# Optimization experiments

Hardware: AMD Instinct MI355X
Metric: run time of the kernel (lower is better)

## Reference

```python
import jax, jax.numpy as jnp
import numpy as np

B, LATENT = 8192, 1024
NR, NC = 12, 12                      # nb_rows, nb_cols
H0, W0 = NR + 2, NC + 2              # 14x14 after reshape
EPS = 1e-5
SLOPE = 0.01                         # LeakyReLU default


def setup_inputs() -> dict:
    key = jax.random.key(0)
    ks = jax.random.split(key, 9)
    s = 0.05
    return {
        "x": jax.random.normal(ks[0], (B, LATENT), jnp.float32),
        "fc_w": jax.random.normal(ks[1], (H0 * W0 * 36, LATENT), jnp.float32) * s,
        "fc_b": jax.random.normal(ks[2], (H0 * W0 * 36,), jnp.float32) * s,
        "conv_w": jax.random.normal(ks[3], (16, 36, 2, 2), jnp.float32) * s,
        "conv_b": jax.random.normal(ks[4], (16,), jnp.float32) * s,
        "gamma": jnp.ones((16,), jnp.float32),
        "beta": jnp.zeros((16,), jnp.float32),
        # locally-connected weights: (out_ch, in_ch, Hout, Wout, k*k)
        "lw1": jax.random.normal(ks[5], (6, 16, H0 - 1, W0 - 1, 4), jnp.float32) * s,
        "lw2": jax.random.normal(ks[6], (1, 6, H0 - 2, W0 - 2, 4), jnp.float32) * s,
    }


def _leaky(x):
    return jnp.where(x >= 0, x, SLOPE * x)


def _local_conv2(x, w):
    # x: (B,C,H,W); w: (O,C,Ho,Wo,4) with k=2, stride 1, no padding
    Ho, Wo = w.shape[2], w.shape[3]
    patches = jnp.stack(
        [x[:, :, dy:dy + Ho, dx:dx + Wo] for dy in (0, 1) for dx in (0, 1)],
        axis=-1)  # (B,C,Ho,Wo,4)
    return jnp.einsum('bchwk,ochwk->bohw', patches, w)


def reference(x, fc_w, fc_b, conv_w, conv_b, gamma, beta, lw1, lw2):
    # fc -> view(B, H0, W0, 36) -> permute to NCHW
    h = x @ fc_w.T + fc_b
    h = h.reshape(B, H0, W0, 36).transpose(0, 3, 1, 2)  # (B,36,14,14)
    # Conv2d k=2 padding='same' (torch pads bottom/right for even kernels)
    h = jax.lax.conv_general_dilated(
        h, conv_w, window_strides=(1, 1), padding=((0, 1), (0, 1)),
        dimension_numbers=('NCHW', 'OIHW', 'NCHW')) + conv_b[None, :, None, None]
    h = _leaky(h)
    # BatchNorm2d (training mode: batch stats, biased var)
    mu = h.mean(axis=(0, 2, 3), keepdims=True)
    var = h.var(axis=(0, 2, 3), keepdims=True)
    h = (h - mu) * jax.lax.rsqrt(var + EPS)
    h = h * gamma[None, :, None, None] + beta[None, :, None, None]
    # locally-connected stack: 14x14 -> 13x13 -> 12x12
    h = _leaky(_local_conv2(h, lw1))
    return _local_conv2(h, lw2)  # (B,1,12,12)
```

## Files before the change

kernel.cpp:

```cpp
#include <hip/hip_runtime.h>


#define SLOPE 0.01f

typedef __bf16 bf16x8 __attribute__((ext_vector_type(8)));
typedef float f32x4 __attribute__((ext_vector_type(4)));

typedef const __attribute__((address_space(1))) void* gas_ptr;
typedef __attribute__((address_space(3))) void* las_ptr;

__device__ __forceinline__ void load16_to_lds(const void* g, void* l) {
  __builtin_amdgcn_global_load_lds((gas_ptr)g, (las_ptr)l, 16, 0, 0);
}

__device__ __forceinline__ unsigned short f2bf(float f) {
  union { float f; unsigned int u; } v; v.f = f;
  unsigned int r = v.u + 0x7FFFu + ((v.u >> 16) & 1u);
  return (unsigned short)(r >> 16);
}
__device__ __forceinline__ float bfbits2f(unsigned int bits16) {
  union { unsigned int u; float f; } v; v.u = bits16 << 16;
  return v.f;
}
__device__ __forceinline__ float leaky(float v) { return v >= 0.f ? v : SLOPE * v; }

__global__ void k_cast_x(const float* __restrict__ x, unsigned short* __restrict__ xb,
                         float* __restrict__ stats) {
  if (blockIdx.x == 0 && threadIdx.x < 32) stats[threadIdx.x] = 0.f;
  int gid = blockIdx.x * 256 + threadIdx.x;
  const float4* x4 = (const float4*)x;
  float4 a = x4[gid * 2], b = x4[gid * 2 + 1];
  union { unsigned short s[8]; uint4 v; } o;
  o.s[0] = f2bf(a.x); o.s[1] = f2bf(a.y); o.s[2] = f2bf(a.z); o.s[3] = f2bf(a.w);
  o.s[4] = f2bf(b.x); o.s[5] = f2bf(b.y); o.s[6] = f2bf(b.z); o.s[7] = f2bf(b.w);
  ((uint4*)xb)[gid] = o.v;
}

__global__ void k_fold(const float* __restrict__ fc_w, const float* __restrict__ fc_b,
                       const float* __restrict__ conv_w, const float* __restrict__ conv_b,
                       unsigned short* __restrict__ Wc, float* __restrict__ bc) {
  __shared__ __align__(16) float cwm[2304];
  int blk = blockIdx.x, t = threadIdx.x;
  if (blk == 196) {
    uint4 z = make_uint4(0, 0, 0, 0);
    uint4* dst = (uint4*)(Wc + 3136 * 1024);
    for (int i = t; i < 8192; i += 256) dst[i] = z;
    for (int i = 3136 + t; i < 3200; i += 256) bc[i] = 0.f;
    return;
  }
  int i0 = blk / 14, j0 = blk - (blk / 14) * 14;
  float m[4];
  int rb[4];
#pragma unroll
  for (int kk = 0; kk < 4; kk++) {
    int dy = kk >> 1, dx = kk & 1;
    int ii = i0 + dy, jj = j0 + dx;
    m[kk] = (ii <= 13 && jj <= 13) ? 1.f : 0.f;
    int iic = ii > 13 ? 13 : ii, jjc = jj > 13 ? 13 : jj;
    rb[kk] = (iic * 14 + jjc) * 36;
  }
  for (int i = t; i < 2304; i += 256) cwm[i] = conv_w[i] * m[i & 3];
  __syncthreads();

  f32x4 acc[16];
#pragma unroll
  for (int o = 0; o < 16; o++) acc[o] = (f32x4){0.f, 0.f, 0.f, 0.f};
  const int kc4 = t * 4;
#pragma unroll 2
  for (int c = 0; c < 36; c++) {
    f32x4 f0 = *(const f32x4*)(fc_w + (rb[0] + c) * 1024 + kc4);
    f32x4 f1 = *(const f32x4*)(fc_w + (rb[1] + c) * 1024 + kc4);
    f32x4 f2 = *(const f32x4*)(fc_w + (rb[2] + c) * 1024 + kc4);
    f32x4 f3 = *(const f32x4*)(fc_w + (rb[3] + c) * 1024 + kc4);
#pragma unroll
    for (int o = 0; o < 16; o++) {
      f32x4 wv = *(const f32x4*)(cwm + (o * 36 + c) * 4);
      acc[o] += wv.x * f0 + wv.y * f1 + wv.z * f2 + wv.w * f3;
    }
  }
#pragma unroll
  for (int o = 0; o < 16; o++) {
    int n = o * 196 + i0 * 14 + j0;
    union { unsigned short s[4]; uint2 v; } u;
    u.s[0] = f2bf(acc[o][0]); u.s[1] = f2bf(acc[o][1]);
    u.s[2] = f2bf(acc[o][2]); u.s[3] = f2bf(acc[o][3]);
    *(uint2*)(Wc + n * 1024 + kc4) = u.v;
  }
  if (t < 16) {
    int o = t;
    float b = conv_b[o];
    for (int c = 0; c < 36; c++)
      for (int dy = 0; dy < 2; dy++) {
        int ii = i0 + dy; if (ii > 13) continue;
        for (int dx = 0; dx < 2; dx++) {
          int jj = j0 + dx; if (jj > 13) continue;
          b += conv_w[(o * 36 + c) * 4 + dy * 2 + dx] * fc_b[(ii * 14 + jj) * 36 + c];
        }
      }
    bc[o * 196 + i0 * 14 + j0] = b;
  }
}

__global__ __launch_bounds__(256, 4) void k_gemm(const unsigned short* __restrict__ Xb,
                                                 const unsigned short* __restrict__ Wcb,
                                                 const float* __restrict__ bc,
                                                 unsigned short* __restrict__ h2,
                                                 float* __restrict__ stats) {
  __shared__ __align__(16) char lds[16384];
  __shared__ float red[4][4];
  const int t = threadIdx.x;
  const int w = t >> 6, lane = t & 63;
  const int quad = lane >> 4, l15 = lane & 15;
  const int bid = blockIdx.x;
  const int xcd = bid & 7, j = bid >> 3;
  const int mblk = xcd * 8 + (j & 7);
  const int nblk = j >> 3;
  const int m0 = mblk * 128, n0 = nblk * 128;
  const int mrow = t & 127, tko = t >> 7;
  const unsigned short* ga = Xb + (m0 + mrow) * 1024 + tko * 8;
  const unsigned short* gb = Wcb + (n0 + mrow) * 1024 + tko * 8;
  char* lA = lds;
  char* lB = lds + 8192;
  const int wbase = w * 1024;
  const int wm0 = (w >> 1) * 64, wn0 = (w & 1) * 64;

  f32x4 acc[4][4];
#pragma unroll
  for (int a = 0; a < 4; a++)
#pragma unroll
    for (int b = 0; b < 4; b++) acc[a][b] = (f32x4){0.f, 0.f, 0.f, 0.f};

  for (int kb = 0; kb < 1024; kb += 32) {
    __syncthreads();
    load16_to_lds(ga + kb,      lA + wbase);
    load16_to_lds(ga + kb + 16, lA + 4096 + wbase);
    load16_to_lds(gb + kb,      lB + wbase);
    load16_to_lds(gb + kb + 16, lB + 4096 + wbase);
    __syncthreads();

    bf16x8 af[4], bfr[4];
#pragma unroll
    for (int mb = 0; mb < 4; mb++)
      af[mb] = *(const bf16x8*)(lA + quad * 2048 + (wm0 + mb * 16 + l15) * 16);
#pragma unroll
    for (int nb = 0; nb < 4; nb++)
      bfr[nb] = *(const bf16x8*)(lB + quad * 2048 + (wn0 + nb * 16 + l15) * 16);
#pragma unroll
    for (int mb = 0; mb < 4; mb++)
#pragma unroll
      for (int nb = 0; nb < 4; nb++)
        acc[mb][nb] = __builtin_amdgcn_mfma_f32_16x16x32_bf16(af[mb], bfr[nb], acc[mb][nb], 0, 0, 0);
  }

  const int cLo = n0 / 196;
  const int cHi = (n0 + 127) / 196;
  float ss0 = 0.f, ss1 = 0.f, sq0 = 0.f, sq1 = 0.f;
#pragma unroll
  for (int nb = 0; nb < 4; nb++) {
    int col = n0 + wn0 + nb * 16 + l15;
    float bias = bc[col];
    int ch = col / 196;
    bool hi = (ch != cLo);
    bool valid = col < 3136;
    float cs = 0.f, cq = 0.f;
#pragma unroll
    for (int mb = 0; mb < 4; mb++) {
#pragma unroll
      for (int r = 0; r < 4; r++) {
        int row = m0 + wm0 + mb * 16 + quad * 4 + r;
        float v = leaky(acc[mb][nb][r] + bias);
        h2[row * 3200 + col] = f2bf(v);
        cs += v; cq += v * v;
      }
    }
    if (valid) {
      if (hi) { ss1 += cs; sq1 += cq; } else { ss0 += cs; sq0 += cq; }
    }
  }
#pragma unroll
  for (int off = 1; off < 64; off <<= 1) {
    ss0 += __shfl_xor(ss0, off, 64);
    ss1 += __shfl_xor(ss1, off, 64);
    sq0 += __shfl_xor(sq0, off, 64);
    sq1 += __shfl_xor(sq1, off, 64);
  }
  if (lane == 0) { red[w][0] = ss0; red[w][1] = ss1; red[w][2] = sq0; red[w][3] = sq1; }
  __syncthreads();
  if (t == 0) {
    float a0 = red[0][0] + red[1][0] + red[2][0] + red[3][0];
    float a1 = red[0][1] + red[1][1] + red[2][1] + red[3][1];
    float b0 = red[0][2] + red[1][2] + red[2][2] + red[3][2];
    float b1 = red[0][3] + red[1][3] + red[2][3] + red[3][3];
    atomicAdd(&stats[cLo], a0);
    atomicAdd(&stats[16 + cLo], b0);
    if (cHi != cLo && cHi < 16) {
      atomicAdd(&stats[cHi], a1);
      atomicAdd(&stats[16 + cHi], b1);
    }
  }
}

__global__ __launch_bounds__(256) void k_tail(const unsigned short* __restrict__ h2,
                                              const float* __restrict__ stats,
                                              const float* __restrict__ gamma,
                                              const float* __restrict__ beta,
                                              const float* __restrict__ lw1,
                                              const float* __restrict__ lw2,
                                              float* __restrict__ out) {
  __shared__ unsigned short h3[4 * 3138];
  __shared__ float h4[4 * 1015];
  __shared__ float sc[16], sh[16];
  int b0 = blockIdx.x * 4, t = threadIdx.x;
  if (t < 16) {
    const float inv = 1.f / 1605632.f;
    float mean = stats[t] * inv;
    float var = stats[16 + t] * inv - mean * mean;
    float rstd = rsqrtf(var + 1e-5f);
    float s = gamma[t] * rstd;
    sc[t] = s; sh[t] = beta[t] - mean * s;
  }
  __syncthreads();
  for (int i = t; i < 6272; i += 256) {
    int bb = i / 1568, q = i - bb * 1568;
    int n = q * 2, o = n / 196;
    unsigned int u = *(const unsigned int*)(h2 + (b0 + bb) * 3200 + n);
    float v0 = bfbits2f(u & 0xffffu) * sc[o] + sh[o];
    float v1 = bfbits2f(u >> 16) * sc[o] + sh[o];
    unsigned int pk = (unsigned int)f2bf(v0) | ((unsigned int)f2bf(v1) << 16);
    *(unsigned int*)(h3 + bb * 3138 + n) = pk;
  }
  __syncthreads();
  for (int u = t; u < 156; u += 256) {
    int rp = u & 1, rest = u >> 1;
    int o = rest / 13, y = rest - o * 13;
    int rA = 2 * rp, rB = 2 * rp + 1;
    float acc0[13], acc1[13];
#pragma unroll
    for (int x = 0; x < 13; x++) { acc0[x] = 0.f; acc1[x] = 0.f; }
    const unsigned short* hA = h3 + rA * 3138;
    const unsigned short* hB = h3 + rB * 3138;
    for (int c = 0; c < 16; c++) {
      float a0[14], a1[14], e0[14], e1[14];
      const unsigned int* pA0 = (const unsigned int*)(hA + c * 196 + y * 14);
      const unsigned int* pA1 = (const unsigned int*)(hA + c * 196 + (y + 1) * 14);
      const unsigned int* pB0 = (const unsigned int*)(hB + c * 196 + y * 14);
      const unsigned int* pB1 = (const unsigned int*)(hB + c * 196 + (y + 1) * 14);
#pragma unroll
      for (int q = 0; q < 7; q++) {
        unsigned int vA0 = pA0[q], vA1 = pA1[q], vB0 = pB0[q], vB1 = pB1[q];
        a0[2 * q] = bfbits2f(vA0 & 0xffffu); a0[2 * q + 1] = bfbits2f(vA0 >> 16);
        a1[2 * q] = bfbits2f(vA1 & 0xffffu); a1[2 * q + 1] = bfbits2f(vA1 >> 16);
        e0[2 * q] = bfbits2f(vB0 & 0xffffu); e0[2 * q + 1] = bfbits2f(vB0 >> 16);
        e1[2 * q] = bfbits2f(vB1 & 0xffffu); e1[2 * q + 1] = bfbits2f(vB1 >> 16);
      }
      const float4* wp4 = (const float4*)(lw1 + (((o * 16 + c) * 13 + y) * 13) * 4);
#pragma unroll
      for (int x = 0; x < 13; x++) {
        float4 wv = wp4[x];
        acc0[x] += a0[x] * wv.x + a0[x + 1] * wv.y + a1[x] * wv.z + a1[x + 1] * wv.w;
        acc1[x] += e0[x] * wv.x + e0[x + 1] * wv.y + e1[x] * wv.z + e1[x + 1] * wv.w;
      }
    }
#pragma unroll
    for (int x = 0; x < 13; x++) {
      h4[rA * 1015 + (o * 13 + y) * 13 + x] = leaky(acc0[x]);
      h4[rB * 1015 + (o * 13 + y) * 13 + x] = leaky(acc1[x]);
    }
  }
  __syncthreads();
  for (int oi = t; oi < 576; oi += 256) {
    int pos = oi >> 2, bb = oi & 3;
    int y = pos / 12, x = pos - y * 12;
    float a = 0.f;
    const float* hp = h4 + bb * 1015;
    const float4* w4 = (const float4*)lw2;
#pragma unroll
    for (int c = 0; c < 6; c++) {
      float4 wv = w4[(c * 12 + y) * 12 + x];
      int hb = c * 169 + y * 13 + x;
      a += hp[hb] * wv.x + hp[hb + 1] * wv.y +
           hp[hb + 13] * wv.z + hp[hb + 14] * wv.w;
    }
    out[(b0 + bb) * 144 + pos] = a;
  }
}

extern "C" void kernel_launch(void* const* d_in, const int* in_sizes, int n_in,
                              void* d_out, int out_size, void* d_ws, size_t ws_size,
                              hipStream_t stream) {
  const float* x      = (const float*)d_in[0];
  const float* fc_w   = (const float*)d_in[1];
  const float* fc_b   = (const float*)d_in[2];
  const float* conv_w = (const float*)d_in[3];
  const float* conv_b = (const float*)d_in[4];
  const float* gamma  = (const float*)d_in[5];
  const float* beta   = (const float*)d_in[6];
  const float* lw1    = (const float*)d_in[7];
  const float* lw2    = (const float*)d_in[8];

  char* ws = (char*)d_ws;
  unsigned short* Xb    = (unsigned short*)(ws);
  unsigned short* Wc    = (unsigned short*)(ws + 16777216);
  float*          bc    = (float*)(ws + 23330816);
  float*          stats = (float*)(ws + 23343616);
  unsigned short* h2    = (unsigned short*)(ws + 23343744);

  k_cast_x<<<4096, 256, 0, stream>>>(x, Xb, stats);
  k_fold<<<197, 256, 0, stream>>>(fc_w, fc_b, conv_w, conv_b, Wc, bc);
  k_gemm<<<1600, 256, 0, stream>>>(Xb, Wc, bc, h2, stats);
  k_tail<<<2048, 256, 0, stream>>>(h2, stats, gamma, beta, lw1, lw2, (float*)d_out);
}
```

Measured before the change: 368.1 us.

## Parallelize tail local-conv across wave lanes and vectorize BN apply loads

```diff
diff --git a/kernel.cpp b/kernel.cpp
--- a/kernel.cpp
+++ b/kernel.cpp
@@ -207,7 +207,7 @@
                                               const float* __restrict__ lw1,
                                               const float* __restrict__ lw2,
                                               float* __restrict__ out) {
-  __shared__ unsigned short h3[4 * 3138];
+  __shared__ __align__(16) unsigned short h3[4 * 3144];
   __shared__ float h4[4 * 1015];
   __shared__ float sc[16], sh[16];
   int b0 = blockIdx.x * 4, t = threadIdx.x;
@@ -220,51 +220,50 @@
     sc[t] = s; sh[t] = beta[t] - mean * s;
   }
   __syncthreads();
-  for (int i = t; i < 6272; i += 256) {
-    int bb = i / 1568, q = i - bb * 1568;
-    int n = q * 2, o = n / 196;
-    unsigned int u = *(const unsigned int*)(h2 + (b0 + bb) * 3200 + n);
-    float v0 = bfbits2f(u & 0xffffu) * sc[o] + sh[o];
-    float v1 = bfbits2f(u >> 16) * sc[o] + sh[o];
-    unsigned int pk = (unsigned int)f2bf(v0) | ((unsigned int)f2bf(v1) << 16);
-    *(unsigned int*)(h3 + bb * 3138 + n) = pk;
-  }
-  __syncthreads();
-  for (int u = t; u < 156; u += 256) {
-    int rp = u & 1, rest = u >> 1;
-    int o = rest / 13, y = rest - o * 13;
-    int rA = 2 * rp, rB = 2 * rp + 1;
-    float acc0[13], acc1[13];
-#pragma unroll
-    for (int x = 0; x < 13; x++) { acc0[x] = 0.f; acc1[x] = 0.f; }
-    const unsigned short* hA = h3 + rA * 3138;
-    const unsigned short* hB = h3 + rB * 3138;
-    for (int c = 0; c < 16; c++) {
-      float a0[14], a1[14], e0[14], e1[14];
-      const unsigned int* pA0 = (const unsigned int*)(hA + c * 196 + y * 14);
-      const unsigned int* pA1 = (const unsigned int*)(hA + c * 196 + (y + 1) * 14);
-      const unsigned int* pB0 = (const unsigned int*)(hB + c * 196 + y * 14);
-      const unsigned int* pB1 = (const unsigned int*)(hB + c * 196 + (y + 1) * 14);
-#pragma unroll
-      for (int q = 0; q < 7; q++) {
-        unsigned int vA0 = pA0[q], vA1 = pA1[q], vB0 = pB0[q], vB1 = pB1[q];
-        a0[2 * q] = bfbits2f(vA0 & 0xffffu); a0[2 * q + 1] = bfbits2f(vA0 >> 16);
-        a1[2 * q] = bfbits2f(vA1 & 0xffffu); a1[2 * q + 1] = bfbits2f(vA1 >> 16);
-        e0[2 * q] = bfbits2f(vB0 & 0xffffu); e0[2 * q + 1] = bfbits2f(vB0 >> 16);
-        e1[2 * q] = bfbits2f(vB1 & 0xffffu); e1[2 * q + 1] = bfbits2f(vB1 >> 16);
+  for (int i = t; i < 1568; i += 256) {
+    int bb = i / 392, q = i - bb * 392;
+    int n = q * 8;
+    uint4 u = *(const uint4*)(h2 + (b0 + bb) * 3200 + n);
+    unsigned int uu[4] = {u.x, u.y, u.z, u.w};
+    unsigned int pk[4];
+#pragma unroll
+    for (int p = 0; p < 4; p++) {
+      int o = (n + 2 * p) / 196;
+      float v0 = bfbits2f(uu[p] & 0xffffu) * sc[o] + sh[o];
+      float v1 = bfbits2f(uu[p] >> 16) * sc[o] + sh[o];
+      pk[p] = (unsigned int)f2bf(v0) | ((unsigned int)f2bf(v1) << 16);
+    }
+    *(uint4*)(h3 + bb * 3144 + n) = make_uint4(pk[0], pk[1], pk[2], pk[3]);
+  }
+  __syncthreads();
+  {
+    int w = t >> 6, lane = t & 63;
+    int c4 = lane >> 4, x = lane & 15;
+    int xc = x > 12 ? 12 : x;
+    for (int u = w; u < 156; u += 4) {
+      int rp = u & 1, rest = u >> 1;
+      int o = rest / 13, y = rest - o * 13;
+      const unsigned short* hA = h3 + (2 * rp) * 3144;
+      const unsigned short* hB = h3 + (2 * rp + 1) * 3144;
+      float accA = 0.f, accB = 0.f;
+#pragma unroll
+      for (int cc = 0; cc < 4; cc++) {
+        int c = c4 * 4 + cc;
+        int base = c * 196 + y * 14 + x;
+        float a0 = bfbits2f(hA[base]);      float a1 = bfbits2f(hA[base + 1]);
+        float a2 = bfbits2f(hA[base + 14]); float a3 = bfbits2f(hA[base + 15]);
+        float e0 = bfbits2f(hB[base]);      float e1 = bfbits2f(hB[base + 1]);
+        float e2 = bfbits2f(hB[base + 14]); float e3 = bfbits2f(hB[base + 15]);
+        float4 wv = *(const float4*)(lw1 + (((o * 16 + c) * 13 + y) * 13 + xc) * 4);
+        accA += a0 * wv.x + a1 * wv.y + a2 * wv.z + a3 * wv.w;
+        accB += e0 * wv.x + e1 * wv.y + e2 * wv.z + e3 * wv.w;
       }
-      const float4* wp4 = (const float4*)(lw1 + (((o * 16 + c) * 13 + y) * 13) * 4);
-#pragma unroll
-      for (int x = 0; x < 13; x++) {
-        float4 wv = wp4[x];
-        acc0[x] += a0[x] * wv.x + a0[x + 1] * wv.y + a1[x] * wv.z + a1[x + 1] * wv.w;
-        acc1[x] += e0[x] * wv.x + e0[x + 1] * wv.y + e1[x] * wv.z + e1[x + 1] * wv.w;
+      accA += __shfl_xor(accA, 16, 64); accA += __shfl_xor(accA, 32, 64);
+      accB += __shfl_xor(accB, 16, 64); accB += __shfl_xor(accB, 32, 64);
+      if (lane < 13) {
+        h4[(2 * rp) * 1015 + (o * 13 + y) * 13 + lane] = leaky(accA);
+        h4[(2 * rp + 1) * 1015 + (o * 13 + y) * 13 + lane] = leaky(accB);
       }
-    }
-#pragma unroll
-    for (int x = 0; x < 13; x++) {
-      h4[rA * 1015 + (o * 13 + y) * 13 + x] = leaky(acc0[x]);
-      h4[rB * 1015 + (o * 13 + y) * 13 + x] = leaky(acc1[x]);
     }
   }
   __syncthreads();
```

After: 544.6 us. 1.48x slower.
